# Performance work log

Hardware: AMD Instinct MI355X
Metric: run time of the kernel (lower is better)

## Reference

```python
import jax, jax.numpy as jnp
import numpy as np

B, S, IN, H, T, OUT = 128, 336, 64, 1024, 96, 1


def _lstm_step(h, c, x, W_ih, W_hh, b_ih, b_hh):
    # PyTorch LSTM cell: gates in (i, f, g, o) order
    g = x @ W_ih.T + b_ih + h @ W_hh.T + b_hh  # [B, 4H]
    i, f, gg, o = jnp.split(g, 4, axis=-1)
    c_new = jax.nn.sigmoid(f) * c + jax.nn.sigmoid(i) * jnp.tanh(gg)
    h_new = jax.nn.sigmoid(o) * jnp.tanh(c_new)
    return h_new, c_new


def setup_inputs() -> dict:
    key = jax.random.key(0)
    ks = jax.random.split(key, 12)
    s = 0.05
    return {
        "src": jax.random.normal(ks[0], (B, S, IN), jnp.float32),
        "enc_W_ih": jax.random.normal(ks[1], (4 * H, IN), jnp.float32) * s,
        "enc_W_hh": jax.random.normal(ks[2], (4 * H, H), jnp.float32) * s,
        "enc_b_ih": jax.random.normal(ks[3], (4 * H,), jnp.float32) * s,
        "enc_b_hh": jax.random.normal(ks[4], (4 * H,), jnp.float32) * s,
        "dec_W_ih": jax.random.normal(ks[5], (4 * H, OUT + H), jnp.float32) * s,
        "dec_W_hh": jax.random.normal(ks[6], (4 * H, H), jnp.float32) * s,
        "dec_b_ih": jax.random.normal(ks[7], (4 * H,), jnp.float32) * s,
        "dec_b_hh": jax.random.normal(ks[8], (4 * H,), jnp.float32) * s,
        "attn_W": jax.random.normal(ks[9], (H, H), jnp.float32) * s,
        "fc_W": jax.random.normal(ks[10], (OUT, H), jnp.float32) * s,
        "fc_b": jax.random.normal(ks[11], (OUT,), jnp.float32) * s,
        "target_len": T,
    }


def reference(src, enc_W_ih, enc_W_hh, enc_b_ih, enc_b_hh,
              dec_W_ih, dec_W_hh, dec_b_ih, dec_b_hh,
              attn_W, fc_W, fc_b, target_len):
    batch = src.shape[0]
    hdim = enc_W_hh.shape[1]

    # ---- Encoder: single-layer LSTM over src, batch_first ----
    def enc_step(carry, x_t):
        h, c = carry
        h, c = _lstm_step(h, c, x_t, enc_W_ih, enc_W_hh, enc_b_ih, enc_b_hh)
        return (h, c), h

    h0 = jnp.zeros((batch, hdim), src.dtype)
    c0 = jnp.zeros((batch, hdim), src.dtype)
    (h_enc, c_enc), enc_hs = jax.lax.scan(enc_step, (h0, c0),
                                          jnp.swapaxes(src, 0, 1))
    encoder_outputs = jnp.swapaxes(enc_hs, 0, 1)  # [B, S, H]

    def dec_step(carry, _):
        h, c, prev_y = carry
        q = h @ attn_W.T                                      # [B, H]
        energy = jnp.einsum('bh,bsh->bs', q, encoder_outputs)  # [B, S]
        w = jax.nn.softmax(energy, axis=-1)
        ctx = jnp.einsum('bs,bsh->bh', w, encoder_outputs)     # [B, H]
        x = jnp.concatenate([prev_y, ctx], axis=-1)            # [B, OUT+H]
        h, c = _lstm_step(h, c, x, dec_W_ih, dec_W_hh, dec_b_ih, dec_b_hh)
        pred = h @ fc_W.T + fc_b                               # [B, OUT]
        prev_y = jax.lax.stop_gradient(pred)                   # pred.detach()
        return (h, c, prev_y), pred

    prev_y0 = jnp.zeros((batch, fc_W.shape[0]), src.dtype)
    _, preds = jax.lax.scan(dec_step, (h_enc, c_enc, prev_y0), None,
                            length=target_len)
    return jnp.swapaxes(preds, 0, 1)  # [B, target_len, OUT]
```

## Files before the change

### kernel.cpp

```cpp
#include <hip/hip_runtime.h>
#include <math.h>

#define Bn   128
#define Sn   336
#define INd  64
#define Hn   1024
#define Tn   96
#define G4   4096
#define KCE  34
#define KCD  65
#define KCQ  32
#define NBLK 256
#define SHALF 168

typedef __attribute__((ext_vector_type(8))) short short8;
typedef __attribute__((ext_vector_type(4))) float floatx4;
typedef __attribute__((ext_vector_type(4))) unsigned int uintx4;
typedef unsigned long long u64t;

__device__ __forceinline__ float sigmoidf_(float x){ return 1.0f/(1.0f+expf(-x)); }

__device__ __forceinline__ unsigned short f2bf(float f){
    union { float f; unsigned u; } v; v.f = f;
    unsigned r = v.u + 0x7fffu + ((v.u >> 16) & 1u);
    return (unsigned short)(r >> 16);
}
__device__ __forceinline__ float bflo(unsigned u){ union{unsigned u; float f;} v; v.u = u << 16;        return v.f; }
__device__ __forceinline__ float bfhi(unsigned u){ union{unsigned u; float f;} v; v.u = u & 0xffff0000u; return v.f; }
__device__ __forceinline__ void unpack8v(uintx4 v, float* f){
    f[0]=bflo(v.x); f[1]=bfhi(v.x); f[2]=bflo(v.y); f[3]=bfhi(v.y);
    f[4]=bflo(v.z); f[5]=bfhi(v.z); f[6]=bflo(v.w); f[7]=bfhi(v.w);
}

union Frag16 { u64t q[2]; short8 s8; uintx4 u4; };
union F2 { u64t q; float f[2]; };

__device__ __forceinline__ short8 ld_cg_s8(const unsigned short* p){
    Frag16 r;
    r.q[0] = __hip_atomic_load((const u64t*)p,     __ATOMIC_RELAXED, __HIP_MEMORY_SCOPE_AGENT);
    r.q[1] = __hip_atomic_load((const u64t*)p + 1, __ATOMIC_RELAXED, __HIP_MEMORY_SCOPE_AGENT);
    return r.s8;
}
__device__ __forceinline__ uintx4 ld_cg_u4(const unsigned short* p){
    Frag16 r;
    r.q[0] = __hip_atomic_load((const u64t*)p,     __ATOMIC_RELAXED, __HIP_MEMORY_SCOPE_AGENT);
    r.q[1] = __hip_atomic_load((const u64t*)p + 1, __ATOMIC_RELAXED, __HIP_MEMORY_SCOPE_AGENT);
    return r.u4;
}
__device__ __forceinline__ void st_cg16(unsigned short* p, unsigned short v){
    asm volatile("global_store_short %0, %1, off sc0 sc1" :: "v"(p), "v"((unsigned)v) : "memory");
}
__device__ __forceinline__ void st_cg32(unsigned short* p, unsigned v){
    asm volatile("global_store_dword %0, %1, off sc0 sc1" :: "v"(p), "v"(v) : "memory");
}
__device__ __forceinline__ void st_cg64(float* p, float a, float b){
    F2 v; v.f[0] = a; v.f[1] = b;
    __hip_atomic_store((u64t*)p, v.q, __ATOMIC_RELAXED, __HIP_MEMORY_SCOPE_AGENT);
}
__device__ __forceinline__ F2 ld_cg64(const float* p){
    F2 v; v.q = __hip_atomic_load((const u64t*)p, __ATOMIC_RELAXED, __HIP_MEMORY_SCOPE_AGENT);
    return v;
}

__device__ __forceinline__ void gbar_full(unsigned* bb, unsigned step){
    asm volatile("s_waitcnt vmcnt(0)" ::: "memory");
    __syncthreads();
    if (threadIdx.x == 0)
        __hip_atomic_store(bb + blockIdx.x*32, step, __ATOMIC_RELAXED, __HIP_MEMORY_SCOPE_AGENT);
    if (blockIdx.x == 0){
        if (threadIdx.x < 64){
            const int l = threadIdx.x;
            for (;;){
                int ok = 1;
                #pragma unroll
                for (int i = 0; i < 4; i++){
                    unsigned a = __hip_atomic_load(bb + (l + i*64)*32,
                                    __ATOMIC_RELAXED, __HIP_MEMORY_SCOPE_AGENT);
                    ok &= (a >= step);
                }
                if (__all(ok)) break;
                __builtin_amdgcn_s_sleep(2);
            }
            #pragma unroll
            for (int i = 0; i < 4; i++)
                __hip_atomic_store(bb + 8192 + (l + i*64)*32, step,
                                   __ATOMIC_RELAXED, __HIP_MEMORY_SCOPE_AGENT);
        }
    } else {
        if (threadIdx.x == 0){
            while (__hip_atomic_load(bb + 8192 + blockIdx.x*32,
                      __ATOMIC_RELAXED, __HIP_MEMORY_SCOPE_AGENT) < step)
                __builtin_amdgcn_s_sleep(2);
        }
    }
    __syncthreads();
}

__device__ __forceinline__ void gbar_grp(unsigned* gb, int gi, unsigned step){
    asm volatile("s_waitcnt vmcnt(0)" ::: "memory");
    __syncthreads();
    if (threadIdx.x == 0)
        __hip_atomic_store(gb + gi*32, step, __ATOMIC_RELAXED, __HIP_MEMORY_SCOPE_AGENT);
    if (gi == 0){
        if (threadIdx.x < 64){
            const int l = threadIdx.x;
            while (__hip_atomic_load(gb + l*32, __ATOMIC_RELAXED,
                                     __HIP_MEMORY_SCOPE_AGENT) < step)
                __builtin_amdgcn_s_sleep(2);
            __hip_atomic_store(gb + 4096 + l*32, step,
                               __ATOMIC_RELAXED, __HIP_MEMORY_SCOPE_AGENT);
        }
    } else {
        if (threadIdx.x == 0){
            while (__hip_atomic_load(gb + 4096 + gi*32, __ATOMIC_RELAXED,
                                     __HIP_MEMORY_SCOPE_AGENT) < step)
                __builtin_amdgcn_s_sleep(2);
        }
    }
    __syncthreads();
}

__global__ void pack_encf(const float* __restrict__ Wih, const float* __restrict__ Whh,
                          const float* __restrict__ bih, const float* __restrict__ bhh,
                          unsigned short* __restrict__ Wp, float* __restrict__ bc){
    long n = (long)256*KCE*512;
    for (long idx = (long)blockIdx.x*256 + threadIdx.x; idx < n; idx += (long)gridDim.x*256){
        int j = (int)(idx & 7), l = (int)((idx >> 3) & 63);
        int kc = (int)((idx >> 9) % KCE);
        int s  = (int)(idx / (KCE*512));
        int c = l & 15, kg = l >> 4;
        int k = kc*32 + kg*8 + j;
        int gate = s & 3, unit = (s >> 2)*16 + c;
        int orig = gate*Hn + unit;
        float v = (k < INd) ? Wih[orig*INd + k] : Whh[(size_t)orig*Hn + (k - INd)];
        Wp[idx] = f2bf(v);
    }
    int tid = blockIdx.x*256 + threadIdx.x;
    if (tid < G4){
        int g = (tid >> 4) & 3, u = (tid >> 6)*16 + (tid & 15);
        int orig = g*Hn + u;
        bc[tid] = bih[orig] + bhh[orig];
    }
}

__global__ void pack_decf(const float* __restrict__ Wih, const float* __restrict__ Whh,
                          const float* __restrict__ bih, const float* __restrict__ bhh,
                          unsigned short* __restrict__ Wp, float* __restrict__ bc){
    long n = (long)256*KCD*512;
    for (long idx = (long)blockIdx.x*256 + threadIdx.x; idx < n; idx += (long)gridDim.x*256){
        int j = (int)(idx & 7), l = (int)((idx >> 3) & 63);
        int kc = (int)((idx >> 9) % KCD);
        int s  = (int)(idx / (KCD*512));
        int c = l & 15, kg = l >> 4;
        int k = kc*32 + kg*8 + j;
        int gate = s & 3, unit = (s >> 2)*16 + c;
        int orig = gate*Hn + unit;
        float v;
        if (k < Hn)          v = Wih[(size_t)orig*(Hn+1) + 1 + k];
        else if (k < 2*Hn)   v = Whh[(size_t)orig*Hn + (k - Hn)];
        else if (k == 2*Hn)  v = Wih[(size_t)orig*(Hn+1)];
        else                 v = 0.0f;
        Wp[idx] = f2bf(v);
    }
    int tid = blockIdx.x*256 + threadIdx.x;
    if (tid < G4){
        int g = (tid >> 4) & 3, u = (tid >> 6)*16 + (tid & 15);
        int orig = g*Hn + u;
        bc[tid] = bih[orig] + bhh[orig];
    }
}

__global__ void pack_attnf(const float* __restrict__ w, unsigned short* __restrict__ Wp){
    int n = 64*KCQ*512;
    for (int idx = blockIdx.x*256 + threadIdx.x; idx < n; idx += gridDim.x*256){
        int j = idx & 7, l = (idx >> 3) & 63;
        int kc = (idx >> 9) & 31;
        int s  = idx >> 14;
        int nn = s*16 + (l & 15);
        int k = kc*32 + (l >> 4)*8 + j;
        Wp[idx] = f2bf(w[(size_t)nn*Hn + k]);
    }
}

__global__ void conv_srcf(const float* __restrict__ s, unsigned short* __restrict__ d){
    int n = Sn*8*2*512;
    for (int idx = blockIdx.x*256 + threadIdx.x; idx < n; idx += gridDim.x*256){
        int j = idx & 7, l = (idx >> 3) & 63;
        int kc = (idx >> 9) & 1, rg = (idx >> 10) & 7, t = idx >> 13;
        int b = rg*16 + (l & 15);
        int k = kc*32 + (l >> 4)*8 + j;
        d[idx] = f2bf(s[((size_t)b*Sn + t)*INd + k]);
    }
}

__global__ void init_ws(unsigned short* __restrict__ hf0, float* __restrict__ cbuf,
                        unsigned short* __restrict__ A0, unsigned short* __restrict__ A1,
                        unsigned* __restrict__ bars, unsigned* __restrict__ pcnt){
    int t0 = blockIdx.x*256 + threadIdx.x;
    for (int i = t0; i < 8*KCD*512; i += gridDim.x*256){
        A0[i] = 0; A1[i] = 0;
        if (i < 8*32*512) hf0[i] = 0;
        if (i < Bn*Hn) cbuf[i] = 0.0f;
        if (i < 49152) bars[i] = 0;
        if (i < 4096)  pcnt[i] = 0;
    }
}

__device__ __forceinline__ void swz(int b, int& x, int& y){
    int xcd = b & 7, li = b >> 3;
    y = xcd*8 + (li & 7);
    x = li >> 3;
}

__device__ __forceinline__ float fcdot(const unsigned short* __restrict__ hplain,
                                       const float* __restrict__ fcW, int b, int l){
    const unsigned short* hp = hplain + (size_t)b*Hn + l*16;
    uintx4 h0 = ld_cg_u4(hp), h1 = ld_cg_u4(hp + 8);
    float hf[16]; unpack8v(h0, hf); unpack8v(h1, hf + 8);
    float p = 0.0f;
    #pragma unroll
    for (int i = 0; i < 16; i++) p = fmaf(hf[i], fcW[l*16 + i], p);
    #pragma unroll
    for (int off = 32; off; off >>= 1) p += __shfl_down(p, off);
    return p;
}

__global__ __launch_bounds__(256, 1)
void enc_loop(const unsigned short* __restrict__ srcfrag,
              const unsigned short* __restrict__ Wf,
              const float* __restrict__ bc, float* __restrict__ cbuf,
              unsigned short* __restrict__ hf0,
              unsigned short* __restrict__ hf1,
              unsigned short* __restrict__ enco,
              unsigned short* __restrict__ adec0,
              unsigned* __restrict__ bar)
{
    __shared__ float red[2][16][65];
    const int tid = threadIdx.x, l = tid & 63, w = tid >> 6;
    const int rgw = w & 1, kh = w >> 1;
    int x, y; swz(blockIdx.x, x, y);
    unsigned* gb = bar + x*8192;
    const int gi = y;
    const int rg = x*2 + rgw;
    const int m0 = rg*16;
    const unsigned short* Bf = Wf + (size_t)(4*y)*KCE*512 + l*8;

    const int col = l & 15, q = l >> 4;
    const int u = y*16 + col;
    const float bi  = bc[y*64 + col];
    const float bf_ = bc[y*64 + 16 + col];
    const float bg  = bc[y*64 + 32 + col];
    const float bo  = bc[y*64 + 48 + col];
    const int lsh = ((u >> 3) & 3) * 16;

    unsigned bstep = 0;
    for (int t = 0; t < Sn; t++){
        const unsigned short* hin = (t & 1) ? hf1 : hf0;
        unsigned short* hout      = (t & 1) ? hf0 : hf1;
        const unsigned short* Ah = hin + (size_t)rg*32*512 + l*8;
        floatx4 acc0={0,0,0,0}, acc1={0,0,0,0}, acc2={0,0,0,0}, acc3={0,0,0,0};

        if (kh == 0){
            short8 ah[15];
            #pragma unroll
            for (int hc = 0; hc < 15; hc++) ah[hc] = ld_cg_s8(Ah + hc*512);
            const unsigned short* Ax = srcfrag + ((size_t)t*8 + rg)*2*512 + l*8;
            #pragma unroll
            for (int kc = 0; kc < 2; kc++){
                short8 a  = *(const short8*)(Ax + kc*512);
                short8 b0 = *(const short8*)(Bf + (0*KCE + kc)*512);
                short8 b1 = *(const short8*)(Bf + (1*KCE + kc)*512);
                short8 b2 = *(const short8*)(Bf + (2*KCE + kc)*512);
                short8 b3 = *(const short8*)(Bf + (3*KCE + kc)*512);
                acc0 = __builtin_amdgcn_mfma_f32_16x16x32_bf16(a, b0, acc0, 0, 0, 0);
                acc1 = __builtin_amdgcn_mfma_f32_16x16x32_bf16(a, b1, acc1, 0, 0, 0);
                acc2 = __builtin_amdgcn_mfma_f32_16x16x32_bf16(a, b2, acc2, 0, 0, 0);
                acc3 = __builtin_amdgcn_mfma_f32_16x16x32_bf16(a, b3, acc3, 0, 0, 0);
            }
            #pragma unroll
            for (int hc = 0; hc < 15; hc++){
                short8 b0 = *(const short8*)(Bf + (0*KCE + hc + 2)*512);
                short8 b1 = *(const short8*)(Bf + (1*KCE + hc + 2)*512);
                short8 b2 = *(const short8*)(Bf + (2*KCE + hc + 2)*512);
                short8 b3 = *(const short8*)(Bf + (3*KCE + hc + 2)*512);
                acc0 = __builtin_amdgcn_mfma_f32_16x16x32_bf16(ah[hc], b0, acc0, 0, 0, 0);
                acc1 = __builtin_amdgcn_mfma_f32_16x16x32_bf16(ah[hc], b1, acc1, 0, 0, 0);
                acc2 = __builtin_amdgcn_mfma_f32_16x16x32_bf16(ah[hc], b2, acc2, 0, 0, 0);
                acc3 = __builtin_amdgcn_mfma_f32_16x16x32_bf16(ah[hc], b3, acc3, 0, 0, 0);
            }
        } else {
            short8 ah[17];
            #pragma unroll
            for (int i = 0; i < 17; i++) ah[i] = ld_cg_s8(Ah + (15 + i)*512);
            #pragma unroll
            for (int i = 0; i < 17; i++){
                short8 b0 = *(const short8*)(Bf + (0*KCE + i + 17)*512);
                short8 b1 = *(const short8*)(Bf + (1*KCE + i + 17)*512);
                short8 b2 = *(const short8*)(Bf + (2*KCE + i + 17)*512);
                short8 b3 = *(const short8*)(Bf + (3*KCE + i + 17)*512);
                acc0 = __builtin_amdgcn_mfma_f32_16x16x32_bf16(ah[i], b0, acc0, 0, 0, 0);
                acc1 = __builtin_amdgcn_mfma_f32_16x16x32_bf16(ah[i], b1, acc1, 0, 0, 0);
                acc2 = __builtin_amdgcn_mfma_f32_16x16x32_bf16(ah[i], b2, acc2, 0, 0, 0);
                acc3 = __builtin_amdgcn_mfma_f32_16x16x32_bf16(ah[i], b3, acc3, 0, 0, 0);
            }
            #pragma unroll
            for (int r = 0; r < 4; r++){
                red[rgw][ 0 + r][l] = acc0[r];
                red[rgw][ 4 + r][l] = acc1[r];
                red[rgw][ 8 + r][l] = acc2[r];
                red[rgw][12 + r][l] = acc3[r];
            }
        }
        __syncthreads();
        if (kh == 0){
            #pragma unroll
            for (int r = 0; r < 4; r++){
                acc0[r] += red[rgw][ 0 + r][l];
                acc1[r] += red[rgw][ 4 + r][l];
                acc2[r] += red[rgw][ 8 + r][l];
                acc3[r] += red[rgw][12 + r][l];
            }
            #pragma unroll
            for (int r = 0; r < 4; r++){
                const int m = m0 + q*4 + r;
                float gi_ = acc0[r] + bi;
                float gf = acc1[r] + bf_;
                float gg = acc2[r] + bg;
                float go = acc3[r] + bo;
                float co = cbuf[(size_t)m*Hn + u];
                float cn = sigmoidf_(gf)*co + sigmoidf_(gi_)*tanhf(gg);
                float hv = sigmoidf_(go)*tanhf(cn);
                cbuf[(size_t)m*Hn + u] = cn;
                unsigned short hb = f2bf(hv);
                const int lanep = (q*4 + r) + lsh;
                st_cg16(hout + (((size_t)rg*32 + (u >> 5))*64 + lanep)*8 + (u & 7), hb);
                enco[((size_t)m*Sn + t)*Hn + u] = hb;
                if (t == Sn-1) adec0[(((size_t)rg*KCD + 32 + (u >> 5))*64 + lanep)*8 + (u & 7)] = hb;
            }
        }
        bstep++; gbar_grp(gb, gi, bstep);
    }
}

__global__ __launch_bounds__(1024, 4)
void dec_loop(unsigned short* __restrict__ A0, unsigned short* __restrict__ A1,
              const unsigned short* __restrict__ Wdec,
              const float* __restrict__ bdec, float* __restrict__ cbuf,
              const unsigned short* __restrict__ Watt,
              unsigned short* __restrict__ qbf,
              const unsigned short* __restrict__ enco,
              unsigned short* __restrict__ hplain,
              float* __restrict__ pctx,
              float* __restrict__ pml,
              unsigned* __restrict__ pcnt,
              const float* __restrict__ fcW, const float* __restrict__ fcb,
              float* __restrict__ out, unsigned* __restrict__ bar)
{
    __shared__ float smem[8224];
    __shared__ unsigned cflag_s;
    const int tid = threadIdx.x, l = tid & 63, w = tid >> 6;
    const int rgw = w & 1, ks = w >> 1;
    int x, y; swz(blockIdx.x, x, y);
    const int rg = x*2 + rgw, m0 = rg*16;
    const unsigned short* Bf = Wdec + (size_t)(4*y)*KCD*512 + l*8;
    const unsigned short* Bq = Watt + (size_t)y*KCQ*512 + l*8;

    const int col = l & 15, q4 = l >> 4;
    const int u = y*16 + col;
    const float bi  = bdec[y*64 + col];
    const float bf_ = bdec[y*64 + 16 + col];
    const float bg  = bdec[y*64 + 32 + col];
    const float bo  = bdec[y*64 + 48 + col];
    const int lsh = ((u >> 3) & 3) * 16;
    const int ab   = blockIdx.x & 127;
    const int part = blockIdx.x >> 7;

    unsigned bstep = 0;
    for (int d = 0; d < Tn; d++){
        unsigned short* Ac = (d & 1) ? A1 : A0;
        unsigned short* An = (d & 1) ? A0 : A1;
        const unsigned short* Af = Ac + (size_t)rg*KCD*512 + l*8;

        floatx4 acc0={0,0,0,0}, acc1={0,0,0,0}, acc2={0,0,0,0}, acc3={0,0,0,0};
        if (w < 8){
            short8 aA[8];
            #pragma unroll
            for (int kk = 0; kk < 8; kk++)
                aA[kk] = ld_cg_s8(Af + (32 + ks*8 + kk)*512);
            floatx4 qa = {0,0,0,0};
            #pragma unroll
            for (int kk = 0; kk < 8; kk++){
                const int kc = 32 + ks*8 + kk;
                short8 b0 = *(const short8*)(Bf + (0*KCD + kc)*512);
                short8 b1 = *(const short8*)(Bf + (1*KCD + kc)*512);
                short8 b2 = *(const short8*)(Bf + (2*KCD + kc)*512);
                short8 b3 = *(const short8*)(Bf + (3*KCD + kc)*512);
                short8 bq = *(const short8*)(Bq + (ks*8 + kk)*512);
                acc0 = __builtin_amdgcn_mfma_f32_16x16x32_bf16(aA[kk], b0, acc0, 0, 0, 0);
                acc1 = __builtin_amdgcn_mfma_f32_16x16x32_bf16(aA[kk], b1, acc1, 0, 0, 0);
                acc2 = __builtin_amdgcn_mfma_f32_16x16x32_bf16(aA[kk], b2, acc2, 0, 0, 0);
                acc3 = __builtin_amdgcn_mfma_f32_16x16x32_bf16(aA[kk], b3, acc3, 0, 0, 0);
                qa   = __builtin_amdgcn_mfma_f32_16x16x32_bf16(aA[kk], bq, qa, 0, 0, 0);
            }
            #pragma unroll
            for (int r = 0; r < 4; r++) smem[(w*4 + r)*64 + l] = qa[r];
        }
        if (d > 0 && x == 0 && w >= 14){
            const int b = y*2 + (w & 1);
            float p = fcdot(hplain, fcW, b, l);
            if (l == 0){
                float pv = p + fcb[0];
                out[b*Tn + (d-1)] = pv;
                st_cg16(Ac + (((size_t)(b >> 4))*KCD + 64)*512 + (b & 15)*8, f2bf(pv));
            }
        }
        __syncthreads();
        if (w < 8 && ks == 0){
            #pragma unroll
            for (int r = 0; r < 4; r++){
                float s = smem[((0*2+rgw)*4 + r)*64 + l] + smem[((1*2+rgw)*4 + r)*64 + l]
                        + smem[((2*2+rgw)*4 + r)*64 + l] + smem[((3*2+rgw)*4 + r)*64 + l];
                st_cg16(qbf + (size_t)(m0 + q4*4 + r)*Hn + y*16 + col, f2bf(s));
            }
        }
        bstep++; gbar_full(bar, bstep);

        {
            float* ctxl = smem;
            float* mred = smem + 8192;
            float* lred = smem + 8208;
            float qv[16];
            {
                const unsigned short* qp = qbf + (size_t)ab*Hn + l*16;
                uintx4 q0 = ld_cg_u4(qp), q1 = ld_cg_u4(qp + 8);
                unpack8v(q0, qv); unpack8v(q1, qv + 8);
            }
            float mx = -1e30f, lsum = 0.0f;
            float cacc[16];
            #pragma unroll
            for (int i = 0; i < 16; i++) cacc[i] = 0.0f;

            const uintx4* ebase = (const uintx4*)(enco + (size_t)ab*Sn*Hn) + l*2;
            const int s0i = part*SHALF;
            for (int s = s0i + w; s < s0i + SHALF; s += 16){
                uintx4 e0 = ebase[(size_t)s*128];
                uintx4 e1 = ebase[(size_t)s*128 + 1];
                float ev[16];
                unpack8v(e0, ev); unpack8v(e1, ev + 8);
                float pt = 0.0f;
                #pragma unroll
                for (int i = 0; i < 16; i++) pt = fmaf(qv[i], ev[i], pt);
                #pragma unroll
                for (int off = 32; off; off >>= 1) pt += __shfl_down(pt, off);
                float e = __shfl(pt, 0);
                float mn = fmaxf(mx, e);
                float corr = expf(mx - mn);
                float p = expf(e - mn);
                lsum = lsum*corr + p;
                if (corr != 1.0f){
                    #pragma unroll
                    for (int i = 0; i < 16; i++) cacc[i] *= corr;
                }
                #pragma unroll
                for (int i = 0; i < 16; i++) cacc[i] = fmaf(p, ev[i], cacc[i]);
                mx = mn;
            }
            if (l == 0){ mred[w] = mx; lred[w] = lsum; }
            __syncthreads();
            float M = mred[0];
            #pragma unroll
            for (int k = 1; k < 16; k++) M = fmaxf(M, mred[k]);
            float corr2 = expf(mx - M);
            if (w < 8){
                #pragma unroll
                for (int j = 0; j < 16; j++) ctxl[w*1024 + j*64 + l] = cacc[j]*corr2;
            }
            __syncthreads();
            if (w >= 8){
                #pragma unroll
                for (int j = 0; j < 16; j++) ctxl[(w-8)*1024 + j*64 + l] += cacc[j]*corr2;
            }
            __syncthreads();
            float L = 0.0f;
            #pragma unroll
            for (int k = 0; k < 16; k++) L += lred[k]*expf(mred[k] - M);

            if (tid < 512){
                const int u0 = 2*tid;
                float s0 = 0.0f, s1 = 0.0f;
                #pragma unroll
                for (int k = 0; k < 8; k++){
                    s0 += ctxl[k*1024 + (u0 & 15)*64 + (u0 >> 4)];
                    s1 += ctxl[k*1024 + ((u0+1) & 15)*64 + ((u0+1) >> 4)];
                }
                st_cg64(pctx + ((size_t)part*128 + ab)*1024 + u0, s0, s1);
            }
            if (tid == 0) st_cg64(pml + ((size_t)part*128 + ab)*2, M, L);

            asm volatile("s_waitcnt vmcnt(0)" ::: "memory");
            __syncthreads();
            if (tid == 0){
                unsigned old = __hip_atomic_fetch_add(pcnt + ab*32, 1u,
                                  __ATOMIC_RELAXED, __HIP_MEMORY_SCOPE_AGENT);
                cflag_s = (old == 2u*(unsigned)d + 1u);
            }
            __syncthreads();
            if (cflag_s && tid < 512){
                const int u0 = 2*tid;
                F2 ml0 = ld_cg64(pml + (size_t)ab*2);
                F2 ml1 = ld_cg64(pml + (size_t)(128 + ab)*2);
                float Mg = fmaxf(ml0.f[0], ml1.f[0]);
                float w0 = expf(ml0.f[0] - Mg), w1 = expf(ml1.f[0] - Mg);
                float invL = 1.0f / (ml0.f[1]*w0 + ml1.f[1]*w1);
                F2 c0 = ld_cg64(pctx + (size_t)ab*1024 + u0);
                F2 c1 = ld_cg64(pctx + ((size_t)128 + ab)*1024 + u0);
                float v0 = (c0.f[0]*w0 + c1.f[0]*w1)*invL;
                float v1 = (c0.f[1]*w0 + c1.f[1]*w1)*invL;
                unsigned cvu = (unsigned)f2bf(v0) | ((unsigned)f2bf(v1) << 16);
                const int kcw = u0 >> 5;
                const int lanep2 = (ab & 15) + ((u0 >> 3) & 3)*16;
                st_cg32(Ac + ((((size_t)(ab >> 4))*KCD + kcw)*64 + lanep2)*8 + (u0 & 7), cvu);
            }
        }
        bstep++; gbar_full(bar, bstep);

        if (w < 8){
            short8 aC[8];
            #pragma unroll
            for (int kk = 0; kk < 8; kk++)
                aC[kk] = ld_cg_s8(Af + (ks*8 + kk)*512);
            #pragma unroll
            for (int kk = 0; kk < 8; kk++){
                const int kc = ks*8 + kk;
                short8 b0 = *(const short8*)(Bf + (0*KCD + kc)*512);
                short8 b1 = *(const short8*)(Bf + (1*KCD + kc)*512);
                short8 b2 = *(const short8*)(Bf + (2*KCD + kc)*512);
                short8 b3 = *(const short8*)(Bf + (3*KCD + kc)*512);
                acc0 = __builtin_amdgcn_mfma_f32_16x16x32_bf16(aC[kk], b0, acc0, 0, 0, 0);
                acc1 = __builtin_amdgcn_mfma_f32_16x16x32_bf16(aC[kk], b1, acc1, 0, 0, 0);
                acc2 = __builtin_amdgcn_mfma_f32_16x16x32_bf16(aC[kk], b2, acc2, 0, 0, 0);
                acc3 = __builtin_amdgcn_mfma_f32_16x16x32_bf16(aC[kk], b3, acc3, 0, 0, 0);
            }
            if (ks == 3){
                short8 a  = ld_cg_s8(Af + 64*512);
                short8 b0 = *(const short8*)(Bf + (0*KCD + 64)*512);
                short8 b1 = *(const short8*)(Bf + (1*KCD + 64)*512);
                short8 b2 = *(const short8*)(Bf + (2*KCD + 64)*512);
                short8 b3 = *(const short8*)(Bf + (3*KCD + 64)*512);
                acc0 = __builtin_amdgcn_mfma_f32_16x16x32_bf16(a, b0, acc0, 0, 0, 0);
                acc1 = __builtin_amdgcn_mfma_f32_16x16x32_bf16(a, b1, acc1, 0, 0, 0);
                acc2 = __builtin_amdgcn_mfma_f32_16x16x32_bf16(a, b2, acc2, 0, 0, 0);
                acc3 = __builtin_amdgcn_mfma_f32_16x16x32_bf16(a, b3, acc3, 0, 0, 0);
            }
            if (ks != 0){
                float* rp = smem + ((ks-1)*2 + rgw)*1024;
                #pragma unroll
                for (int r = 0; r < 4; r++){
                    rp[( 0 + r)*64 + l] = acc0[r];
                    rp[( 4 + r)*64 + l] = acc1[r];
                    rp[( 8 + r)*64 + l] = acc2[r];
                    rp[(12 + r)*64 + l] = acc3[r];
                }
            }
        }
        __syncthreads();
        if (w < 8 && ks == 0){
            const float* r0 = smem + rgw*1024;
            const float* r1 = smem + (2 + rgw)*1024;
            const float* r2 = smem + (4 + rgw)*1024;
            #pragma unroll
            for (int r = 0; r < 4; r++){
                acc0[r] += r0[( 0+r)*64 + l] + r1[( 0+r)*64 + l] + r2[( 0+r)*64 + l];
                acc1[r] += r0[( 4+r)*64 + l] + r1[( 4+r)*64 + l] + r2[( 4+r)*64 + l];
                acc2[r] += r0[( 8+r)*64 + l] + r1[( 8+r)*64 + l] + r2[( 8+r)*64 + l];
                acc3[r] += r0[(12+r)*64 + l] + r1[(12+r)*64 + l] + r2[(12+r)*64 + l];
            }
            #pragma unroll
            for (int r = 0; r < 4; r++){
                const int m = m0 + q4*4 + r;
                float gi = acc0[r] + bi;
                float gf = acc1[r] + bf_;
                float gg = acc2[r] + bg;
                float go = acc3[r] + bo;
                float co = cbuf[(size_t)m*Hn + u];
                float cn = sigmoidf_(gf)*co + sigmoidf_(gi)*tanhf(gg);
                float hv = sigmoidf_(go)*tanhf(cn);
                cbuf[(size_t)m*Hn + u] = cn;
                unsigned short hb = f2bf(hv);
                const int lanep = (q4*4 + r) + lsh;
                st_cg16(An + (((size_t)rg*KCD + 32 + (u >> 5))*64 + lanep)*8 + (u & 7), hb);
                st_cg16(hplain + (size_t)m*Hn + u, hb);
            }
        }
        bstep++; gbar_full(bar, bstep);
    }

    if (x == 0 && w >= 14){
        const int b = y*2 + (w & 1);
        float p = fcdot(hplain, fcW, b, l);
        if (l == 0) out[b*Tn + (Tn - 1)] = p + fcb[0];
    }
}

extern "C" void kernel_launch(void* const* d_in, const int* in_sizes, int n_in,
                              void* d_out, int out_size, void* d_ws, size_t ws_size,
                              hipStream_t stream){
    const float* src  = (const float*)d_in[0];
    const float* eWih = (const float*)d_in[1];
    const float* eWhh = (const float*)d_in[2];
    const float* ebih = (const float*)d_in[3];
    const float* ebhh = (const float*)d_in[4];
    const float* dWih = (const float*)d_in[5];
    const float* dWhh = (const float*)d_in[6];
    const float* dbih = (const float*)d_in[7];
    const float* dbhh = (const float*)d_in[8];
    const float* attnW= (const float*)d_in[9];
    const float* fcW  = (const float*)d_in[10];
    const float* fcb  = (const float*)d_in[11];
    float* out = (float*)d_out;

    char* base = (char*)d_ws;
    auto alloc = [&](size_t bytes){ void* p = base; base += (bytes + 255) & ~255ull; return p; };
    unsigned short* Wencf = (unsigned short*)alloc((size_t)256*KCE*512*2);
    float*          benc  = (float*)alloc(G4*4);
    unsigned short* Wdecf = (unsigned short*)alloc((size_t)256*KCD*512*2);
    float*          bdec  = (float*)alloc(G4*4);
    unsigned short* Wattf = (unsigned short*)alloc((size_t)64*KCQ*512*2);
    unsigned short* srcf  = (unsigned short*)alloc((size_t)Sn*8*2*512*2);
    unsigned short* enco  = (unsigned short*)alloc((size_t)Bn*Sn*Hn*2);
    unsigned short* hf0   = (unsigned short*)alloc((size_t)8*32*512*2);
    unsigned short* hf1   = (unsigned short*)alloc((size_t)8*32*512*2);
    float*          cbuf  = (float*)alloc((size_t)Bn*Hn*4);
    unsigned short* A0f   = (unsigned short*)alloc((size_t)8*KCD*512*2);
    unsigned short* A1f   = (unsigned short*)alloc((size_t)8*KCD*512*2);
    unsigned short* qbf   = (unsigned short*)alloc((size_t)Bn*Hn*2);
    unsigned short* hplain= (unsigned short*)alloc((size_t)Bn*Hn*2);
    float*          pctx  = (float*)alloc((size_t)2*128*1024*4);
    float*          pml   = (float*)alloc((size_t)2*128*2*4);
    unsigned*       bars  = (unsigned*)alloc((size_t)49152*4);
    unsigned*       pcnt  = (unsigned*)alloc((size_t)4096*4);

    conv_srcf<<<2048, 256, 0, stream>>>(src, srcf);
    pack_encf<<<4096, 256, 0, stream>>>(eWih, eWhh, ebih, ebhh, Wencf, benc);
    pack_decf<<<8192, 256, 0, stream>>>(dWih, dWhh, dbih, dbhh, Wdecf, bdec);
    pack_attnf<<<1024, 256, 0, stream>>>(attnW, Wattf);
    init_ws<<<1040, 256, 0, stream>>>(hf0, cbuf, A0f, A1f, bars, pcnt);

    enc_loop<<<NBLK, 256, 0, stream>>>(srcf, Wencf, benc, cbuf, hf0, hf1,
                                       enco, A0f, bars);
    dec_loop<<<NBLK, 1024, 0, stream>>>(A0f, A1f, Wdecf, bdec, cbuf, Wattf,
                                        qbf, enco, hplain, pctx, pml, pcnt,
                                        fcW, fcb, out, bars + 32768);
}
```

Baseline: 11.31 ms.

## Keep decoder encoder-output slice resident in LDS and registers across steps

The decoder kernel now runs 512 threads per block and loads each block's half of the encoder outputs for one batch row once before the time loop. The first 24 rows go to LDS and the remaining 144 rows are held in registers, 18 rows per wave. This removes the per-step global/L2 streaming of encoder outputs in the attention phase. Reductions are reworked into serialized LDS accumulation across 8 waves. The cost is very high register pressure with possible spills, and fewer waves to hide latency in the MFMA phases.

```diff
diff --git a/kernel.cpp b/kernel.cpp
--- a/kernel.cpp
+++ b/kernel.cpp
@@ -12,6 +12,8 @@
 #define KCQ  32
 #define NBLK 256
 #define SHALF 168
+#define LROWS 24
+#define RROWS 18
 
 typedef __attribute__((ext_vector_type(8))) short short8;
 typedef __attribute__((ext_vector_type(4))) float floatx4;
@@ -342,7 +344,21 @@
     }
 }
 
-__global__ __launch_bounds__(1024, 4)
+#define EROW(E0, E1) { \
+    float ev[16]; unpack8v(E0, ev); unpack8v(E1, ev + 8); \
+    float pt = 0.0f; \
+    _Pragma("unroll") for (int i_ = 0; i_ < 16; i_++) pt = fmaf(qv[i_], ev[i_], pt); \
+    _Pragma("unroll") for (int o_ = 32; o_; o_ >>= 1) pt += __shfl_down(pt, o_); \
+    float e_ = __shfl(pt, 0); \
+    float mn_ = fmaxf(mx, e_); \
+    float corr_ = expf(mx - mn_); \
+    float p_ = expf(e_ - mn_); \
+    lsum = lsum*corr_ + p_; \
+    if (corr_ != 1.0f){ _Pragma("unroll") for (int i_ = 0; i_ < 16; i_++) cacc[i_] *= corr_; } \
+    _Pragma("unroll") for (int i_ = 0; i_ < 16; i_++) cacc[i_] = fmaf(p_, ev[i_], cacc[i_]); \
+    mx = mn_; }
+
+__global__ __launch_bounds__(512, 2)
 void dec_loop(unsigned short* __restrict__ A0, unsigned short* __restrict__ A1,
               const unsigned short* __restrict__ Wdec,
               const float* __restrict__ bdec, float* __restrict__ cbuf,
@@ -356,8 +372,11 @@
               const float* __restrict__ fcW, const float* __restrict__ fcb,
               float* __restrict__ out, unsigned* __restrict__ bar)
 {
-    __shared__ float smem[8224];
-    __shared__ unsigned cflag_s;
+    __shared__ __align__(16) unsigned char ldsraw[57600];
+    unsigned short* elds = (unsigned short*)ldsraw;
+    float* scr = (float*)(ldsraw + 49152);
+    unsigned* scru = (unsigned*)scr;
+
     const int tid = threadIdx.x, l = tid & 63, w = tid >> 6;
     const int rgw = w & 1, ks = w >> 1;
     int x, y; swz(blockIdx.x, x, y);
@@ -374,6 +393,24 @@
     const int lsh = ((u >> 3) & 3) * 16;
     const int ab   = blockIdx.x & 127;
     const int part = blockIdx.x >> 7;
+    const int s0i  = part*SHALF;
+
+    {
+        const uintx4* esrc = (const uintx4*)(enco + ((size_t)ab*Sn + s0i)*Hn);
+        for (int i = tid; i < LROWS*128; i += 512)
+            ((uintx4*)elds)[i] = esrc[i];
+    }
+    uintx4 er0[RROWS], er1[RROWS];
+    {
+        const uintx4* ebase = (const uintx4*)(enco + (size_t)ab*Sn*Hn) + l*2;
+        #pragma unroll
+        for (int i = 0; i < RROWS; i++){
+            const size_t s_ = (size_t)(s0i + LROWS + w*RROWS + i);
+            er0[i] = ebase[s_*128];
+            er1[i] = ebase[s_*128 + 1];
+        }
+    }
+    __syncthreads();
 
     unsigned bstep = 0;
     for (int d = 0; d < Tn; d++){
@@ -382,7 +419,7 @@
         const unsigned short* Af = Ac + (size_t)rg*KCD*512 + l*8;
 
         floatx4 acc0={0,0,0,0}, acc1={0,0,0,0}, acc2={0,0,0,0}, acc3={0,0,0,0};
-        if (w < 8){
+        {
             short8 aA[8];
             #pragma unroll
             for (int kk = 0; kk < 8; kk++)
@@ -403,9 +440,9 @@
                 qa   = __builtin_amdgcn_mfma_f32_16x16x32_bf16(aA[kk], bq, qa, 0, 0, 0);
             }
             #pragma unroll
-            for (int r = 0; r < 4; r++) smem[(w*4 + r)*64 + l] = qa[r];
-        }
-        if (d > 0 && x == 0 && w >= 14){
+            for (int r = 0; r < 4; r++) scr[(w*4 + r)*64 + l] = qa[r];
+        }
+        if (d > 0 && x == 0 && w >= 6){
             const int b = y*2 + (w & 1);
             float p = fcdot(hplain, fcW, b, l);
             if (l == 0){
@@ -415,20 +452,17 @@
             }
         }
         __syncthreads();
-        if (w < 8 && ks == 0){
-            #pragma unroll
-            for (int r = 0; r < 4; r++){
-                float s = smem[((0*2+rgw)*4 + r)*64 + l] + smem[((1*2+rgw)*4 + r)*64 + l]
-                        + smem[((2*2+rgw)*4 + r)*64 + l] + smem[((3*2+rgw)*4 + r)*64 + l];
+        if (ks == 0){
+            #pragma unroll
+            for (int r = 0; r < 4; r++){
+                float s = scr[((0*2+rgw)*4 + r)*64 + l] + scr[((1*2+rgw)*4 + r)*64 + l]
+                        + scr[((2*2+rgw)*4 + r)*64 + l] + scr[((3*2+rgw)*4 + r)*64 + l];
                 st_cg16(qbf + (size_t)(m0 + q4*4 + r)*Hn + y*16 + col, f2bf(s));
             }
         }
         bstep++; gbar_full(bar, bstep);
 
         {
-            float* ctxl = smem;
-            float* mred = smem + 8192;
-            float* lred = smem + 8208;
             float qv[16];
             {
                 const unsigned short* qp = qbf + (size_t)ab*Hn + l*16;
@@ -440,61 +474,54 @@
             #pragma unroll
             for (int i = 0; i < 16; i++) cacc[i] = 0.0f;
 
-            const uintx4* ebase = (const uintx4*)(enco + (size_t)ab*Sn*Hn) + l*2;
-            const int s0i = part*SHALF;
-            for (int s = s0i + w; s < s0i + SHALF; s += 16){
-                uintx4 e0 = ebase[(size_t)s*128];
-                uintx4 e1 = ebase[(size_t)s*128 + 1];
-                float ev[16];
-                unpack8v(e0, ev); unpack8v(e1, ev + 8);
-                float pt = 0.0f;
+            #pragma unroll
+            for (int i = 0; i < 3; i++){
+                const unsigned short* rp = elds + (w*3 + i)*1024 + l*16;
+                uintx4 e0 = *(const uintx4*)rp;
+                uintx4 e1 = *(const uintx4*)(rp + 8);
+                EROW(e0, e1)
+            }
+            #pragma unroll
+            for (int i = 0; i < RROWS; i++){
+                EROW(er0[i], er1[i])
+            }
+
+            if (l == 0){ scr[2048 + w] = mx; scr[2064 + w] = lsum; }
+            __syncthreads();
+            float M = scr[2048];
+            #pragma unroll
+            for (int k = 1; k < 8; k++) M = fmaxf(M, scr[2048 + k]);
+            float corr2 = expf(mx - M);
+            if (ks == 0){
                 #pragma unroll
-                for (int i = 0; i < 16; i++) pt = fmaf(qv[i], ev[i], pt);
+                for (int j = 0; j < 16; j++) scr[rgw*1024 + j*64 + l] = cacc[j]*corr2;
+            }
+            __syncthreads();
+            if (ks == 1){
                 #pragma unroll
-                for (int off = 32; off; off >>= 1) pt += __shfl_down(pt, off);
-                float e = __shfl(pt, 0);
-                float mn = fmaxf(mx, e);
-                float corr = expf(mx - mn);
-                float p = expf(e - mn);
-                lsum = lsum*corr + p;
-                if (corr != 1.0f){
-                    #pragma unroll
-                    for (int i = 0; i < 16; i++) cacc[i] *= corr;
-                }
+                for (int j = 0; j < 16; j++) scr[rgw*1024 + j*64 + l] += cacc[j]*corr2;
+            }
+            __syncthreads();
+            if (ks == 2){
                 #pragma unroll
-                for (int i = 0; i < 16; i++) cacc[i] = fmaf(p, ev[i], cacc[i]);
-                mx = mn;
-            }
-            if (l == 0){ mred[w] = mx; lred[w] = lsum; }
+                for (int j = 0; j < 16; j++) scr[rgw*1024 + j*64 + l] += cacc[j]*corr2;
+            }
             __syncthreads();
-            float M = mred[0];
-            #pragma unroll
-            for (int k = 1; k < 16; k++) M = fmaxf(M, mred[k]);
-            float corr2 = expf(mx - M);
-            if (w < 8){
+            if (ks == 3){
                 #pragma unroll
-                for (int j = 0; j < 16; j++) ctxl[w*1024 + j*64 + l] = cacc[j]*corr2;
-            }
-            __syncthreads();
-            if (w >= 8){
-                #pragma unroll
-                for (int j = 0; j < 16; j++) ctxl[(w-8)*1024 + j*64 + l] += cacc[j]*corr2;
+                for (int j = 0; j < 16; j++) scr[rgw*1024 + j*64 + l] += cacc[j]*corr2;
             }
             __syncthreads();
             float L = 0.0f;
             #pragma unroll
-            for (int k = 0; k < 16; k++) L += lred[k]*expf(mred[k] - M);
-
-            if (tid < 512){
-                const int u0 = 2*tid;
-                float s0 = 0.0f, s1 = 0.0f;
-                #pragma unroll
-                for (int k = 0; k < 8; k++){
-                    s0 += ctxl[k*1024 + (u0 & 15)*64 + (u0 >> 4)];
-                    s1 += ctxl[k*1024 + ((u0+1) & 15)*64 + ((u0+1) >> 4)];
-                }
-                st_cg64(pctx + ((size_t)part*128 + ab)*1024 + u0, s0, s1);
-            }
+            for (int k = 0; k < 8; k++) L += scr[2064 + k]*expf(scr[2048 + k] - M);
+
+            const int u0 = 2*tid;
+            float s0 = scr[(u0 & 15)*64 + (u0 >> 4)]
+                     + scr[1024 + (u0 & 15)*64 + (u0 >> 4)];
+            float s1 = scr[((u0+1) & 15)*64 + ((u0+1) >> 4)]
+                     + scr[1024 + ((u0+1) & 15)*64 + ((u0+1) >> 4)];
+            st_cg64(pctx + ((size_t)part*128 + ab)*1024 + u0, s0, s1);
             if (tid == 0) st_cg64(pml + ((size_t)part*128 + ab)*2, M, L);
 
             asm volatile("s_waitcnt vmcnt(0)" ::: "memory");
@@ -502,11 +529,10 @@
             if (tid == 0){
                 unsigned old = __hip_atomic_fetch_add(pcnt + ab*32, 1u,
                                   __ATOMIC_RELAXED, __HIP_MEMORY_SCOPE_AGENT);
-                cflag_s = (old == 2u*(unsigned)d + 1u);
+                scru[2080] = (old == 2u*(unsigned)d + 1u) ? 1u : 0u;
             }
             __syncthreads();
-            if (cflag_s && tid < 512){
-                const int u0 = 2*tid;
+            if (scru[2080]){
                 F2 ml0 = ld_cg64(pml + (size_t)ab*2);
                 F2 ml1 = ld_cg64(pml + (size_t)(128 + ab)*2);
                 float Mg = fmaxf(ml0.f[0], ml1.f[0]);
@@ -524,7 +550,7 @@
         }
         bstep++; gbar_full(bar, bstep);
 
-        if (w < 8){
+        {
             short8 aC[8];
             #pragma unroll
             for (int kk = 0; kk < 8; kk++)
@@ -552,28 +578,48 @@
                 acc2 = __builtin_amdgcn_mfma_f32_16x16x32_bf16(a, b2, acc2, 0, 0, 0);
                 acc3 = __builtin_amdgcn_mfma_f32_16x16x32_bf16(a, b3, acc3, 0, 0, 0);
             }
-            if (ks != 0){
-                float* rp = smem + ((ks-1)*2 + rgw)*1024;
-                #pragma unroll
-                for (int r = 0; r < 4; r++){
-                    rp[( 0 + r)*64 + l] = acc0[r];
-                    rp[( 4 + r)*64 + l] = acc1[r];
-                    rp[( 8 + r)*64 + l] = acc2[r];
-                    rp[(12 + r)*64 + l] = acc3[r];
-                }
+        }
+        if (ks == 1){
+            float* rp = scr + rgw*1024;
+            #pragma unroll
+            for (int r = 0; r < 4; r++){
+                rp[( 0 + r)*64 + l] = acc0[r];
+                rp[( 4 + r)*64 + l] = acc1[r];
+                rp[( 8 + r)*64 + l] = acc2[r];
+                rp[(12 + r)*64 + l] = acc3[r];
             }
         }
         __syncthreads();
-        if (w < 8 && ks == 0){
-            const float* r0 = smem + rgw*1024;
-            const float* r1 = smem + (2 + rgw)*1024;
-            const float* r2 = smem + (4 + rgw)*1024;
-            #pragma unroll
-            for (int r = 0; r < 4; r++){
-                acc0[r] += r0[( 0+r)*64 + l] + r1[( 0+r)*64 + l] + r2[( 0+r)*64 + l];
-                acc1[r] += r0[( 4+r)*64 + l] + r1[( 4+r)*64 + l] + r2[( 4+r)*64 + l];
-                acc2[r] += r0[( 8+r)*64 + l] + r1[( 8+r)*64 + l] + r2[( 8+r)*64 + l];
-                acc3[r] += r0[(12+r)*64 + l] + r1[(12+r)*64 + l] + r2[(12+r)*64 + l];
+        if (ks == 2){
+            float* rp = scr + rgw*1024;
+            #pragma unroll
+            for (int r = 0; r < 4; r++){
+                rp[( 0 + r)*64 + l] += acc0[r];
+                rp[( 4 + r)*64 + l] += acc1[r];
+                rp[( 8 + r)*64 + l] += acc2[r];
+                rp[(12 + r)*64 + l] += acc3[r];
+            }
+        }
+        __syncthreads();
+        if (ks == 3){
+            float* rp = scr + rgw*1024;
+            #pragma unroll
+            for (int r = 0; r < 4; r++){
+                rp[( 0 + r)*64 + l] += acc0[r];
+                rp[( 4 + r)*64 + l] += acc1[r];
+                rp[( 8 + r)*64 + l] += acc2[r];
+                rp[(12 + r)*64 + l] += acc3[r];
+            }
+        }
+        __syncthreads();
+        if (ks == 0){
+            const float* rp = scr + rgw*1024;
+            #pragma unroll
+            for (int r = 0; r < 4; r++){
+                acc0[r] += rp[( 0 + r)*64 + l];
+                acc1[r] += rp[( 4 + r)*64 + l];
+                acc2[r] += rp[( 8 + r)*64 + l];
+                acc3[r] += rp[(12 + r)*64 + l];
             }
             #pragma unroll
             for (int r = 0; r < 4; r++){
@@ -595,7 +641,7 @@
         bstep++; gbar_full(bar, bstep);
     }
 
-    if (x == 0 && w >= 14){
+    if (x == 0 && w >= 6){
         const int b = y*2 + (w & 1);
         float p = fcdot(hplain, fcW, b, l);
         if (l == 0) out[b*Tn + (Tn - 1)] = p + fcb[0];
@@ -648,7 +694,7 @@
 
     enc_loop<<<NBLK, 256, 0, stream>>>(srcf, Wencf, benc, cbuf, hf0, hf1,
                                        enco, A0f, bars);
-    dec_loop<<<NBLK, 1024, 0, stream>>>(A0f, A1f, Wdecf, bdec, cbuf, Wattf,
-                                        qbf, enco, hplain, pctx, pml, pcnt,
-                                        fcW, fcb, out, bars + 32768);
-}
+    dec_loop<<<NBLK, 512, 0, stream>>>(A0f, A1f, Wdecf, bdec, cbuf, Wattf,
+                                       qbf, enco, hplain, pctx, pml, pcnt,
+                                       fcW, fcb, out, bars + 32768);
+}
```

Result: slower. 17.02 ms (+50.6%).
